# Performance work log

Hardware: AMD Instinct MI355X
Metric: run time of the kernel (lower is better)

## Reference

```python
import jax, jax.numpy as jnp
import numpy as np

H, D, EF, NT, ET = 4, 32, 32, 4, 8
N, E = 100000, 1600000
NEG_SLOPE = 0.2


def setup_inputs() -> dict:
    key = jax.random.key(0)
    ks = jax.random.split(key, 11)
    return {
        "feat": jax.random.normal(ks[0], (N, H * D), jnp.float32),
        "fc": jax.random.normal(ks[1], (NT, H, D), jnp.float32) * 0.1,
        "edge_emb": jax.random.normal(ks[2], (ET, EF), jnp.float32),
        "W_e": jax.random.normal(ks[3], (H * EF, EF), jnp.float32) * 0.1,
        "attn_l": jax.random.normal(ks[4], (1, H, D), jnp.float32) * 0.1,
        "attn_r": jax.random.normal(ks[5], (1, H, D), jnp.float32) * 0.1,
        "attn_e": jax.random.normal(ks[6], (1, H, EF), jnp.float32) * 0.1,
        "node_types": jax.random.randint(ks[7], (N,), 0, NT, jnp.int32),
        "e_feat": jax.random.randint(ks[8], (E,), 0, ET, jnp.int32),
        "src": jax.random.randint(ks[9], (E,), 0, N, jnp.int32),
        "dst": jax.random.randint(ks[10], (E,), 0, N, jnp.int32),
    }


def reference(feat, fc, edge_emb, W_e, attn_l, attn_r, attn_e, node_types, e_feat, src, dst):
    n = feat.shape[0]
    h = feat.reshape(n, H, D)                      # [N,H,D] (h_src == h_dst)
    fs = h * fc[node_types]                        # per-node-type scaling, feat_src == feat_dst

    # edge-type embedding path: Embedding -> Linear(edge_feats, H*edge_feats) -> attn_e score
    emb = (edge_emb @ W_e.T).reshape(ET, H, EF)    # [ET,H,EF]
    ee = (emb * attn_e).sum(-1)[e_feat]            # [E,H]

    el = (fs * attn_l).sum(-1)                     # [N,H]
    er = (fs * attn_r).sum(-1)                     # [N,H]
    e = jax.nn.leaky_relu(el[src] + er[dst] + ee, NEG_SLOPE)  # [E,H]

    # edge_softmax: segment softmax over destination node
    m = jax.ops.segment_max(e, dst, num_segments=n)           # [N,H]
    ex = jnp.exp(e - m[dst])
    s = jax.ops.segment_sum(ex, dst, num_segments=n)          # [N,H]
    a = ex / s[dst]                                            # [E,H]

    # u_mul_e + sum aggregation
    msg = fs[src] * a[:, :, None]                              # [E,H,D]
    rst = jax.ops.segment_sum(msg, dst, num_segments=n)       # [N,H,D]

    rst = rst + h                                              # residual (Identity, in==out feats)
    return rst, a[:, :, None]
```

## Files before the change

kernel.cpp:

```cpp
#include <hip/hip_runtime.h>
#include <stdint.h>

namespace {
constexpr int kH = 4, kD = 32, kEF = 32, kNT = 4, kET = 8;
constexpr int kHD = kH * kD;
constexpr float kNegSlope = 0.2f;
constexpr int kBN = 128;
constexpr int kNB = (100000 + kBN - 1) / kBN;
constexpr int kHB = 512;
constexpr int kXP = 20;

using f32x2 = __attribute__((ext_vector_type(2))) float;
using f32x4 = __attribute__((ext_vector_type(4))) float;

__device__ __forceinline__ float lrelu(float x) { return x > 0.f ? x : kNegSlope * x; }

__global__ void __launch_bounds__(256) k_init(
    const float* __restrict__ feat, const float* __restrict__ fc,
    const float* __restrict__ edge_emb, const float* __restrict__ W_e,
    const float* __restrict__ attn_l, const float* __restrict__ attn_r,
    const float* __restrict__ attn_e, const int* __restrict__ node_types,
    float* __restrict__ el, float* __restrict__ ernv, uint8_t* __restrict__ fs,
    float* __restrict__ ee_tab, int N) {
  if (blockIdx.x == 0 && threadIdx.x < kET * kH) {
    int et = threadIdx.x / kH, h = threadIdx.x % kH;
    float acc = 0.f;
    for (int f = 0; f < kEF; ++f) {
      const float* wrow = W_e + (h * kEF + f) * kEF;
      const float* erow = edge_emb + et * kEF;
      float emb = 0.f;
      for (int k = 0; k < kEF; ++k) emb += erow[k] * wrow[k];
      acc += emb * attn_e[h * kEF + f];
    }
    ee_tab[et * kH + h] = acc;
  }
  int gid = blockIdx.x * blockDim.x + threadIdx.x;
  int node = gid >> 5;
  int lane = threadIdx.x & 31;
  if (node >= N) return;
  int nt = node_types[node];
  float4 f4 = *(const float4*)(feat + (size_t)(node << 7) + lane * 4);
  float4 c4 = *(const float4*)(fc + nt * kHD + lane * 4);
  float4 al = *(const float4*)(attn_l + lane * 4);
  float4 ar = *(const float4*)(attn_r + lane * 4);
  float fx = f4.x * c4.x, fy = f4.y * c4.y, fz = f4.z * c4.z, fw = f4.w * c4.w;
  int w = __builtin_amdgcn_cvt_pk_fp8_f32(fx, fy, 0, false);
  w = __builtin_amdgcn_cvt_pk_fp8_f32(fz, fw, w, true);
  *(int*)(fs + (size_t)(node << 7) + lane * 4) = w;
  float pl = fx * al.x + fy * al.y + fz * al.z + fw * al.w;
  float pr = fx * ar.x + fy * ar.y + fz * ar.z + fw * ar.w;
#pragma unroll
  for (int off = 1; off < 8; off <<= 1) {
    pl += __shfl_xor(pl, off);
    pr += __shfl_xor(pr, off);
  }
  if ((lane & 7) == 0) {
    int h = lane >> 3;
    el[node * kH + h] = pl;
    ernv[(node << 3) + h] = pr;
  }
}

__global__ void __launch_bounds__(256) k_hist(const int* __restrict__ dst,
                                              int* __restrict__ partial, int E) {
  __shared__ int h[kNB];
  for (int i = threadIdx.x; i < kNB; i += 256) h[i] = 0;
  __syncthreads();
  int per = (E + gridDim.x - 1) / gridDim.x;
  int e0 = blockIdx.x * per;
  int e1 = min(e0 + per, E);
  for (int i = e0 + threadIdx.x; i < e1; i += 256) atomicAdd(&h[dst[i] >> 7], 1);
  __syncthreads();
  for (int i = threadIdx.x; i < kNB; i += 256) partial[blockIdx.x * kNB + i] = h[i];
}

__global__ void __launch_bounds__(256) k_scanA(int* __restrict__ partial,
                                               int* __restrict__ btot) {
  __shared__ int bufa[kHB], bufb[kHB];
  int b = blockIdx.x, t = threadIdx.x;
  bufa[t] = partial[t * kNB + b];
  bufa[t + 256] = partial[(t + 256) * kNB + b];
  __syncthreads();
  int* cur = bufa;
  int* nxt = bufb;
  for (int off = 1; off < kHB; off <<= 1) {
    for (int i = t; i < kHB; i += 256) nxt[i] = cur[i] + (i >= off ? cur[i - off] : 0);
    __syncthreads();
    int* sw = cur; cur = nxt; nxt = sw;
  }
  partial[t * kNB + b] = t ? cur[t - 1] : 0;
  partial[(t + 256) * kNB + b] = cur[t + 255];
  if (t == 0) btot[b] = cur[kHB - 1];
}

__global__ void __launch_bounds__(256) k_scatter2(
    const int* __restrict__ dst, const int* __restrict__ src,
    const int* __restrict__ e_feat, const int* __restrict__ partial,
    const int* __restrict__ btot, int* __restrict__ tmp, int E) {
  __shared__ int h[kNB], sA[kNB], sB[kNB], bb[kNB];
  int t = threadIdx.x;
  for (int i = t; i < kNB; i += 256) sA[i] = btot[i];
  __syncthreads();
  int* cur = sA;
  int* nxt = sB;
  for (int off = 1; off < kNB; off <<= 1) {
    for (int i = t; i < kNB; i += 256) nxt[i] = cur[i] + (i >= off ? cur[i - off] : 0);
    __syncthreads();
    int* sw = cur; cur = nxt; nxt = sw;
  }
  for (int i = t; i < kNB; i += 256) {
    bb[i] = i ? cur[i - 1] : 0;
    h[i] = 0;
  }
  __syncthreads();
  int per = (E + gridDim.x - 1) / gridDim.x;
  int e0 = blockIdx.x * per;
  int e1 = min(e0 + per, E);
  const int* myrow = partial + blockIdx.x * kNB;
  for (int i = e0 + t; i < e1; i += 256) {
    int d = dst[i];
    int b = d >> 7;
    int lr = atomicAdd(&h[b], 1);
    int pos = bb[b] + myrow[b] + lr;
    tmp[pos] = src[i] | (e_feat[i] << 17) | ((d & 127) << 20);
  }
}

__global__ void __launch_bounds__(256) k_build(const int* __restrict__ btot,
                                               const int* __restrict__ tmp,
                                               int* __restrict__ ptr,
                                               int* __restrict__ csr, int N, int E) {
  __shared__ int fh[128], fb[128], sc[128];
  __shared__ int red[256];
  int b = blockIdx.x, t = threadIdx.x;
  int acc = 0;
  for (int i = t; i < b; i += 256) acc += btot[i];
  red[t] = acc;
  __syncthreads();
  for (int off = 128; off > 0; off >>= 1) {
    if (t < off) red[t] += red[t + off];
    __syncthreads();
  }
  int s0 = red[0];
  int s1 = s0 + btot[b];
  if (t < 128) fh[t] = 0;
  __syncthreads();
  for (int j = s0 + t; j < s1; j += 256) atomicAdd(&fh[tmp[j] >> 20], 1);
  __syncthreads();
  if (t < 128) sc[t] = fh[t];
  __syncthreads();
  for (int off = 1; off < 128; off <<= 1) {
    int v = 0;
    if (t < 128 && t >= off) v = sc[t - off];
    __syncthreads();
    if (t < 128) sc[t] += v;
    __syncthreads();
  }
  if (t < 128) {
    fb[t] = sc[t] - fh[t];
    int d = (b << 7) + t;
    if (d < N) ptr[d] = s0 + fb[t];
    fh[t] = 0;
  }
  if (b == gridDim.x - 1 && t == 0) ptr[N] = E;
  __syncthreads();
  for (int j = s0 + t; j < s1; j += 256) {
    int v = tmp[j];
    int dl = v >> 20;
    int r = atomicAdd(&fh[dl], 1);
    csr[s0 + fb[dl] + r] = v & 0xFFFFF;
  }
}

__global__ void __launch_bounds__(256) k_fused(
    const uint8_t* __restrict__ fs, const float* __restrict__ feat,
    const float* __restrict__ el, float* __restrict__ ernv,
    const float* __restrict__ ee_tab, const int* __restrict__ ptr,
    const int* __restrict__ csr, float* __restrict__ rst, int N) {
  __shared__ float ee_sh[kET * kH];
  __shared__ __align__(16) float xp[4][64 * kXP];
  if (threadIdx.x < kET * kH) ee_sh[threadIdx.x] = ee_tab[threadIdx.x];
  __syncthreads();
  int lane = threadIdx.x & 63;
  int wid = threadIdx.x >> 6;
  int node = blockIdx.x * 4 + wid;
  if (node >= N) return;
  int start = ptr[node], end = ptr[node + 1];

  int g = lane >> 3;
  int q = lane & 7;
  int head = q >> 1;
  int qoff = q << 4;
  float er_h = ernv[(node << 3) + head];
  f32x2 f2 = *(const f32x2*)(feat + ((size_t)node << 7) + lane * 2);

  float sm = 0.f;
  f32x2 acc[8];
#pragma unroll
  for (int k = 0; k < 8; ++k) acc[k] = (f32x2){0.f, 0.f};

  int j = start + g;
  int pk0 = csr[(j < end) ? j : 0];
  int pk1 = csr[(j + 8 < end) ? j + 8 : 0];
  int s0 = pk0 & 0x1FFFF;
  float elv0 = el[(s0 << 2) + head];
  int4 w0 = *(const int4*)(fs + ((size_t)s0 << 7) + qoff);
  float ee0 = ee_sh[((pk0 >> 17) << 2) + head];
  int s1 = pk1 & 0x1FFFF;
  float elv1 = el[(s1 << 2) + head];
  int4 w1 = *(const int4*)(fs + ((size_t)s1 << 7) + qoff);
  float ee1 = ee_sh[((pk1 >> 17) << 2) + head];
  int pk2 = csr[(j + 16 < end) ? j + 16 : 0];

  while (j < end) {
    int s2 = pk2 & 0x1FFFF;
    float elv2 = el[(s2 << 2) + head];
    int4 w2 = *(const int4*)(fs + ((size_t)s2 << 7) + qoff);
    float ee2 = ee_sh[((pk2 >> 17) << 2) + head];
    int pk3 = csr[(j + 24 < end) ? j + 24 : 0];
    float ex = __expf(lrelu(elv0 + er_h + ee0));
    sm += ex;
    f32x2 ex2 = {ex, ex};
#pragma unroll
    for (int c = 0; c < 4; ++c) {
      int wc = c == 0 ? w0.x : c == 1 ? w0.y : c == 2 ? w0.z : w0.w;
      acc[2 * c + 0] += ex2 * __builtin_amdgcn_cvt_pk_f32_fp8(wc, false);
      acc[2 * c + 1] += ex2 * __builtin_amdgcn_cvt_pk_f32_fp8(wc, true);
    }
    elv0 = elv1; w0 = w1; ee0 = ee1;
    elv1 = elv2; w1 = w2; ee1 = ee2;
    pk2 = pk3;
    j += 8;
  }

  sm += __shfl_xor(sm, 8);
  sm += __shfl_xor(sm, 16);
  sm += __shfl_xor(sm, 32);
  float rinv = sm > 0.f ? 1.f / sm : 0.f;

  float* row = &xp[wid][lane * kXP];
#pragma unroll
  for (int c = 0; c < 4; ++c) {
    float4 v4 = {acc[2 * c].x, acc[2 * c].y, acc[2 * c + 1].x, acc[2 * c + 1].y};
    *(float4*)(row + c * 4) = v4;
  }
  asm volatile("s_waitcnt lgkmcnt(0)" ::: "memory");
  __builtin_amdgcn_sched_barrier(0);
  int qsrc = lane >> 3;
  int coff = (lane & 7) * 2;
  const float* base = &xp[wid][qsrc * kXP + coff];
  f32x2 v = {0.f, 0.f};
#pragma unroll
  for (int gg = 0; gg < 8; ++gg) v += *(const f32x2*)(base + gg * 8 * kXP);

  float rs = __shfl(rinv, (lane >> 4) << 1);
  float rb = __shfl(rinv, lane << 1);
  f32x2 o = v * rs + f2;
  __builtin_nontemporal_store(o, (f32x2*)(rst + ((size_t)node << 7) + lane * 2));
  if (lane < kH) ernv[(node << 3) + 4 + lane] = rb;
}

__global__ void __launch_bounds__(256) k_post(
    const int* __restrict__ src, const int* __restrict__ dst,
    const int* __restrict__ e_feat, const float* __restrict__ el,
    const float* __restrict__ ernv, const float* __restrict__ ee_tab,
    float* __restrict__ out_a, int E) {
  int i = blockIdx.x * blockDim.x + threadIdx.x;
  if (i >= E) return;
  int s = src[i], d = dst[i], et = e_feat[i];
  float4 elv = *(const float4*)(el + s * kH);
  float4 erv = *(const float4*)(ernv + ((size_t)d << 3));
  float4 rv = *(const float4*)(ernv + ((size_t)d << 3) + 4);
  float4 ee = *(const float4*)(ee_tab + et * kH);
  f32x4 a;
  a.x = __expf(lrelu(elv.x + erv.x + ee.x)) * rv.x;
  a.y = __expf(lrelu(elv.y + erv.y + ee.y)) * rv.y;
  a.z = __expf(lrelu(elv.z + erv.z + ee.z)) * rv.z;
  a.w = __expf(lrelu(elv.w + erv.w + ee.w)) * rv.w;
  __builtin_nontemporal_store(a, (f32x4*)(out_a + (size_t)i * kH));
}

}

extern "C" void kernel_launch(void* const* d_in, const int* in_sizes, int n_in,
                              void* d_out, int out_size, void* d_ws, size_t ws_size,
                              hipStream_t stream) {
  const float* feat = (const float*)d_in[0];
  const float* fc = (const float*)d_in[1];
  const float* edge_emb = (const float*)d_in[2];
  const float* W_e = (const float*)d_in[3];
  const float* attn_l = (const float*)d_in[4];
  const float* attn_r = (const float*)d_in[5];
  const float* attn_e = (const float*)d_in[6];
  const int* node_types = (const int*)d_in[7];
  const int* e_feat = (const int*)d_in[8];
  const int* src = (const int*)d_in[9];
  const int* dst = (const int*)d_in[10];
  int N = in_sizes[7];
  int E = in_sizes[8];

  char* ws = (char*)d_ws;
  size_t off = 0;
  auto alloc = [&](size_t bytes) -> void* {
    void* p = ws + off;
    off = (off + bytes + 255) & ~(size_t)255;
    return p;
  };
  float* ee_tab = (float*)alloc((size_t)kET * kH * sizeof(float));
  float* el = (float*)alloc((size_t)N * kH * sizeof(float));
  float* ernv = (float*)alloc((size_t)N * 2 * kH * sizeof(float));
  uint8_t* fs = (uint8_t*)alloc((size_t)N * kHD * sizeof(uint8_t));
  int* partial = (int*)alloc((size_t)kHB * kNB * sizeof(int));
  int* btot = (int*)alloc((size_t)kNB * sizeof(int));
  int* ptr = (int*)alloc((size_t)(N + 1) * sizeof(int));
  int* tmp = (int*)alloc((size_t)E * sizeof(int));
  int* csr = (int*)alloc((size_t)E * sizeof(int));

  k_init<<<(N + 7) / 8, 256, 0, stream>>>(feat, fc, edge_emb, W_e, attn_l, attn_r,
                                          attn_e, node_types, el, ernv, fs, ee_tab, N);
  k_hist<<<kHB, 256, 0, stream>>>(dst, partial, E);
  k_scanA<<<kNB, 256, 0, stream>>>(partial, btot);
  k_scatter2<<<kHB, 256, 0, stream>>>(dst, src, e_feat, partial, btot, tmp, E);
  k_build<<<kNB, 256, 0, stream>>>(btot, tmp, ptr, csr, N, E);

  float* rst = (float*)d_out;
  float* out_a = (float*)d_out + (size_t)N * kHD;
  k_fused<<<(N + 3) / 4, 256, 0, stream>>>(fs, feat, el, ernv, ee_tab, ptr, csr,
                                           rst, N);
  k_post<<<(E + 255) / 256, 256, 0, stream>>>(src, dst, e_feat, el, ernv, ee_tab,
                                              out_a, E);
}
```

Measured before the change: 303.2 us.

## Fuse CSR build kernels into one cooperative kernel with grid syncs

Replaces the separate histogram, scan, scatter and build kernels with a single cooperative kernel that uses grid-wide barriers between phases. The per-block partial-count matrix and its column scan are replaced by global atomic bucket totals plus an atomic cursor that hands each block its offset in every bucket. This removes three kernel launches and the partial-matrix memory traffic. In exchange it adds grid-sync overhead and atomic contention, and the edge order inside each bucket is no longer deterministic.

```diff
diff --git a/kernel.cpp b/kernel.cpp
--- a/kernel.cpp
+++ b/kernel.cpp
@@ -1,5 +1,8 @@
 #include <hip/hip_runtime.h>
+#include <hip/hip_cooperative_groups.h>
 #include <stdint.h>
+
+namespace cg = cooperative_groups;
 
 namespace {
 constexpr int kH = 4, kD = 32, kEF = 32, kNT = 4, kET = 8;
@@ -7,7 +10,7 @@
 constexpr float kNegSlope = 0.2f;
 constexpr int kBN = 128;
 constexpr int kNB = (100000 + kBN - 1) / kBN;
-constexpr int kHB = 512;
+constexpr int kSB = 512;
 constexpr int kXP = 20;
 
 using f32x2 = __attribute__((ext_vector_type(2))) float;
@@ -61,44 +64,34 @@
   }
 }
 
-__global__ void __launch_bounds__(256) k_hist(const int* __restrict__ dst,
-                                              int* __restrict__ partial, int E) {
-  __shared__ int h[kNB];
-  for (int i = threadIdx.x; i < kNB; i += 256) h[i] = 0;
-  __syncthreads();
-  int per = (E + gridDim.x - 1) / gridDim.x;
+__global__ void __launch_bounds__(256, 4) k_sort(
+    const int* __restrict__ dst, const int* __restrict__ src,
+    const int* __restrict__ e_feat, int* __restrict__ btot,
+    int* __restrict__ cursor, int* __restrict__ tmp, int* __restrict__ ptr,
+    int* __restrict__ csr, int N, int E) {
+  __shared__ int h[kNB], r[kNB], sA[kNB], sB[kNB];
+  __shared__ int fh[kBN], fb[kBN], sc[kBN];
+  cg::grid_group grid = cg::this_grid();
+  int t = threadIdx.x;
+  int nblk = gridDim.x;
+  int gtid = blockIdx.x * 256 + t;
+
+  for (int i = gtid; i < kNB; i += nblk * 256) {
+    btot[i] = 0;
+    cursor[i] = 0;
+  }
+  for (int i = t; i < kNB; i += 256) h[i] = 0;
+  __syncthreads();
+  int per = (E + nblk - 1) / nblk;
   int e0 = blockIdx.x * per;
   int e1 = min(e0 + per, E);
-  for (int i = e0 + threadIdx.x; i < e1; i += 256) atomicAdd(&h[dst[i] >> 7], 1);
-  __syncthreads();
-  for (int i = threadIdx.x; i < kNB; i += 256) partial[blockIdx.x * kNB + i] = h[i];
-}
-
-__global__ void __launch_bounds__(256) k_scanA(int* __restrict__ partial,
-                                               int* __restrict__ btot) {
-  __shared__ int bufa[kHB], bufb[kHB];
-  int b = blockIdx.x, t = threadIdx.x;
-  bufa[t] = partial[t * kNB + b];
-  bufa[t + 256] = partial[(t + 256) * kNB + b];
-  __syncthreads();
-  int* cur = bufa;
-  int* nxt = bufb;
-  for (int off = 1; off < kHB; off <<= 1) {
-    for (int i = t; i < kHB; i += 256) nxt[i] = cur[i] + (i >= off ? cur[i - off] : 0);
-    __syncthreads();
-    int* sw = cur; cur = nxt; nxt = sw;
-  }
-  partial[t * kNB + b] = t ? cur[t - 1] : 0;
-  partial[(t + 256) * kNB + b] = cur[t + 255];
-  if (t == 0) btot[b] = cur[kHB - 1];
-}
-
-__global__ void __launch_bounds__(256) k_scatter2(
-    const int* __restrict__ dst, const int* __restrict__ src,
-    const int* __restrict__ e_feat, const int* __restrict__ partial,
-    const int* __restrict__ btot, int* __restrict__ tmp, int E) {
-  __shared__ int h[kNB], sA[kNB], sB[kNB], bb[kNB];
-  int t = threadIdx.x;
+  for (int i = e0 + t; i < e1; i += 256) atomicAdd(&h[dst[i] >> 7], 1);
+  __syncthreads();
+  grid.sync();
+  for (int i = t; i < kNB; i += 256)
+    if (h[i]) atomicAdd(&btot[i], h[i]);
+  grid.sync();
+
   for (int i = t; i < kNB; i += 256) sA[i] = btot[i];
   __syncthreads();
   int* cur = sA;
@@ -109,66 +102,50 @@
     int* sw = cur; cur = nxt; nxt = sw;
   }
   for (int i = t; i < kNB; i += 256) {
-    bb[i] = i ? cur[i - 1] : 0;
-    h[i] = 0;
-  }
-  __syncthreads();
-  int per = (E + gridDim.x - 1) / gridDim.x;
-  int e0 = blockIdx.x * per;
-  int e1 = min(e0 + per, E);
-  const int* myrow = partial + blockIdx.x * kNB;
+    int bbv = i ? cur[i - 1] : 0;
+    int cnt = h[i];
+    r[i] = bbv + (cnt ? atomicAdd(&cursor[i], cnt) : 0);
+  }
+  __syncthreads();
   for (int i = e0 + t; i < e1; i += 256) {
     int d = dst[i];
     int b = d >> 7;
-    int lr = atomicAdd(&h[b], 1);
-    int pos = bb[b] + myrow[b] + lr;
+    int pos = atomicAdd(&r[b], 1);
     tmp[pos] = src[i] | (e_feat[i] << 17) | ((d & 127) << 20);
   }
-}
-
-__global__ void __launch_bounds__(256) k_build(const int* __restrict__ btot,
-                                               const int* __restrict__ tmp,
-                                               int* __restrict__ ptr,
-                                               int* __restrict__ csr, int N, int E) {
-  __shared__ int fh[128], fb[128], sc[128];
-  __shared__ int red[256];
-  int b = blockIdx.x, t = threadIdx.x;
-  int acc = 0;
-  for (int i = t; i < b; i += 256) acc += btot[i];
-  red[t] = acc;
-  __syncthreads();
-  for (int off = 128; off > 0; off >>= 1) {
-    if (t < off) red[t] += red[t + off];
-    __syncthreads();
-  }
-  int s0 = red[0];
-  int s1 = s0 + btot[b];
-  if (t < 128) fh[t] = 0;
-  __syncthreads();
-  for (int j = s0 + t; j < s1; j += 256) atomicAdd(&fh[tmp[j] >> 20], 1);
-  __syncthreads();
-  if (t < 128) sc[t] = fh[t];
-  __syncthreads();
-  for (int off = 1; off < 128; off <<= 1) {
-    int v = 0;
-    if (t < 128 && t >= off) v = sc[t - off];
-    __syncthreads();
-    if (t < 128) sc[t] += v;
-    __syncthreads();
-  }
-  if (t < 128) {
-    fb[t] = sc[t] - fh[t];
-    int d = (b << 7) + t;
-    if (d < N) ptr[d] = s0 + fb[t];
-    fh[t] = 0;
-  }
-  if (b == gridDim.x - 1 && t == 0) ptr[N] = E;
-  __syncthreads();
-  for (int j = s0 + t; j < s1; j += 256) {
-    int v = tmp[j];
-    int dl = v >> 20;
-    int r = atomicAdd(&fh[dl], 1);
-    csr[s0 + fb[dl] + r] = v & 0xFFFFF;
+  grid.sync();
+
+  for (int b = blockIdx.x; b < kNB; b += nblk) {
+    int s0 = b ? cur[b - 1] : 0;
+    int s1 = s0 + btot[b];
+    if (t < kBN) fh[t] = 0;
+    __syncthreads();
+    for (int j = s0 + t; j < s1; j += 256) atomicAdd(&fh[tmp[j] >> 20], 1);
+    __syncthreads();
+    if (t < kBN) sc[t] = fh[t];
+    __syncthreads();
+    for (int off = 1; off < kBN; off <<= 1) {
+      int v = 0;
+      if (t < kBN && t >= off) v = sc[t - off];
+      __syncthreads();
+      if (t < kBN) sc[t] += v;
+      __syncthreads();
+    }
+    if (t < kBN) {
+      fb[t] = sc[t] - fh[t];
+      int d = (b << 7) + t;
+      if (d < N) ptr[d] = s0 + fb[t];
+      fh[t] = 0;
+    }
+    if (b == kNB - 1 && t == 0) ptr[N] = E;
+    __syncthreads();
+    for (int j = s0 + t; j < s1; j += 256) {
+      int v = tmp[j];
+      int dl = v >> 20;
+      int rr = atomicAdd(&fh[dl], 1);
+      csr[s0 + fb[dl] + rr] = v & 0xFFFFF;
+    }
+    __syncthreads();
   }
 }
 
@@ -310,18 +287,21 @@
   float* el = (float*)alloc((size_t)N * kH * sizeof(float));
   float* ernv = (float*)alloc((size_t)N * 2 * kH * sizeof(float));
   uint8_t* fs = (uint8_t*)alloc((size_t)N * kHD * sizeof(uint8_t));
-  int* partial = (int*)alloc((size_t)kHB * kNB * sizeof(int));
   int* btot = (int*)alloc((size_t)kNB * sizeof(int));
+  int* cursor = (int*)alloc((size_t)kNB * sizeof(int));
   int* ptr = (int*)alloc((size_t)(N + 1) * sizeof(int));
   int* tmp = (int*)alloc((size_t)E * sizeof(int));
   int* csr = (int*)alloc((size_t)E * sizeof(int));
 
   k_init<<<(N + 7) / 8, 256, 0, stream>>>(feat, fc, edge_emb, W_e, attn_l, attn_r,
                                           attn_e, node_types, el, ernv, fs, ee_tab, N);
-  k_hist<<<kHB, 256, 0, stream>>>(dst, partial, E);
-  k_scanA<<<kNB, 256, 0, stream>>>(partial, btot);
-  k_scatter2<<<kHB, 256, 0, stream>>>(dst, src, e_feat, partial, btot, tmp, E);
-  k_build<<<kNB, 256, 0, stream>>>(btot, tmp, ptr, csr, N, E);
+
+  {
+    void* args[] = {(void*)&dst, (void*)&src, (void*)&e_feat, (void*)&btot,
+                    (void*)&cursor, (void*)&tmp, (void*)&ptr, (void*)&csr,
+                    (void*)&N, (void*)&E};
+    hipLaunchCooperativeKernel((void*)k_sort, dim3(kSB), dim3(256), args, 0, stream);
+  }
 
   float* rst = (float*)d_out;
   float* out_a = (float*)d_out + (size_t)N * kHD;
```

Result: slower. 481.2 us (+58.7%).
